# Kernel tuning notes

Measured on AMD Instinct MI355X. Metric: run time of the kernel, lower is better.

Reference implementation:

```python
import jax, jax.numpy as jnp
import numpy as np

B, C, F = 8, 2048, 128


def setup_inputs() -> dict:
    key = jax.random.key(0)
    ks = jax.random.split(key, 13)
    features = jax.random.normal(ks[0], (B, C, F), dtype=jnp.float32)
    # sparse-ish boolean adjacency masks over operations
    pred_mask = jax.random.uniform(ks[1], (B, C, C)) < 0.05
    succ_mask = jax.random.uniform(ks[2], (B, C, C)) < 0.05
    same_type_mask = jax.random.uniform(ks[3], (B, C, C)) < 0.10

    def linear(k, fan_in, fan_out):
        kw, kb = jax.random.split(k)
        bound = 1.0 / np.sqrt(fan_in)
        W = jax.random.uniform(kw, (fan_in, fan_out), minval=-bound, maxval=bound, dtype=jnp.float32)
        b = jax.random.uniform(kb, (fan_out,), minval=-bound, maxval=bound, dtype=jnp.float32)
        return W, b

    W_enc, b_enc = linear(ks[4], F, 4 * F)
    W_space, b_space = linear(ks[5], 3 * F, F)
    W_same, b_same = linear(ks[6], 2 * F, F)
    W_mix, b_mix = linear(ks[7], 2 * F, F)
    return {
        "features": features,
        "pred_mask": pred_mask,
        "succ_mask": succ_mask,
        "same_type_mask": same_type_mask,
        "W_enc": W_enc, "b_enc": b_enc,
        "W_space": W_space, "b_space": b_space,
        "W_same": W_same, "b_same": b_same,
        "W_mix": W_mix, "b_mix": b_mix,
    }


def reference(features, pred_mask, succ_mask, same_type_mask,
              W_enc, b_enc, W_space, b_space, W_same, b_same, W_mix, b_mix):
    # encoder: [B,C,F] -> [B,C,4F], split into origin + 3 message features
    enc = features @ W_enc + b_enc
    origin, e_pred, e_succ, e_same = jnp.split(enc, 4, axis=-1)

    def masked_mean(mask, e):
        # original builds (B,C,C,F) broadcast product then sums over 'other';
        # mathematically this is mask @ e with a clamped-degree divisor.
        m = mask.astype(e.dtype)                         # [B,C,C]
        deg = jnp.maximum(m.sum(-1, keepdims=True), 1.0)  # [B,C,1]
        return jnp.einsum('bij,bjf->bif', m, e) / deg

    pred_f = masked_mean(pred_mask, e_pred)
    succ_f = masked_mean(succ_mask, e_succ)
    same_f = masked_mean(same_type_mask, e_same)

    space_mixed = jnp.concatenate([pred_f, origin, succ_f], axis=-1) @ W_space + b_space
    same_mixed = jnp.concatenate([origin, same_f], axis=-1) @ W_same + b_same
    return jnp.concatenate([space_mixed, same_mixed], axis=-1) @ W_mix + b_mix
```

## Files before the change

### kernel.cpp

```cpp
#include <hip/hip_runtime.h>
#include <stdint.h>

typedef unsigned int uint;
typedef unsigned short ushort;
typedef unsigned char uchar;
typedef __attribute__((ext_vector_type(8))) short bf16x8;
typedef __attribute__((ext_vector_type(4))) float f32x4;

__device__ __forceinline__ ushort f2bf(float f) {
  uint u = __builtin_bit_cast(uint, f);
  return (ushort)((u + 0x7FFFu + ((u >> 16) & 1u)) >> 16);
}

__device__ __forceinline__ bf16x8 cvt8(uint lo, uint hi, uint& cacc) {
  uint x0 = __builtin_amdgcn_perm(0u, lo, 0x04010400u);
  uint x1 = __builtin_amdgcn_perm(0u, lo, 0x04030402u);
  uint x2 = __builtin_amdgcn_perm(0u, hi, 0x04010400u);
  uint x3 = __builtin_amdgcn_perm(0u, hi, 0x04030402u);
  uint n0 = ((x0 + 0x00FF00FFu) >> 8) & 0x00010001u;
  uint n1 = ((x1 + 0x00FF00FFu) >> 8) & 0x00010001u;
  uint n2 = ((x2 + 0x00FF00FFu) >> 8) & 0x00010001u;
  uint n3 = ((x3 + 0x00FF00FFu) >> 8) & 0x00010001u;
  cacc += n0 + n1 + n2 + n3;
  uint4 o;
  o.x = n0 * 0x3F80u; o.y = n1 * 0x3F80u;
  o.z = n2 * 0x3F80u; o.w = n3 * 0x3F80u;
  return __builtin_bit_cast(bf16x8, o);
}

__device__ __forceinline__ bf16x8 cvt8w(uint4 a, uint4 b, uint& cnt) {
  bf16x8 r;
  r[0] = a.x ? (short)0x3F80 : (short)0; cnt += (a.x != 0u);
  r[1] = a.y ? (short)0x3F80 : (short)0; cnt += (a.y != 0u);
  r[2] = a.z ? (short)0x3F80 : (short)0; cnt += (a.z != 0u);
  r[3] = a.w ? (short)0x3F80 : (short)0; cnt += (a.w != 0u);
  r[4] = b.x ? (short)0x3F80 : (short)0; cnt += (b.x != 0u);
  r[5] = b.y ? (short)0x3F80 : (short)0; cnt += (b.y != 0u);
  r[6] = b.z ? (short)0x3F80 : (short)0; cnt += (b.z != 0u);
  r[7] = b.w ? (short)0x3F80 : (short)0; cnt += (b.w != 0u);
  return r;
}

__global__ __launch_bounds__(256) void k_detect(
    const uint4* __restrict__ m, int* __restrict__ esz_out) {
  __shared__ int s_ok;
  if (threadIdx.x == 0) s_ok = 1;
  __syncthreads();
  int ok = 1;
#pragma unroll
  for (int i = 0; i < 16; ++i) {
    uint4 v = m[i * 256 + threadIdx.x];
    if (!(v.x <= 1u || v.x == 0x3F800000u)) ok = 0;
    if (!(v.y <= 1u || v.y == 0x3F800000u)) ok = 0;
    if (!(v.z <= 1u || v.z == 0x3F800000u)) ok = 0;
    if (!(v.w <= 1u || v.w == 0x3F800000u)) ok = 0;
  }
  if (!ok) atomicAnd(&s_ok, 0);
  __syncthreads();
  if (threadIdx.x == 0) *esz_out = s_ok ? 4 : 1;
}

__global__ __launch_bounds__(256) void k_prep(
    const float4* __restrict__ fin, ushort* __restrict__ fout,
    const float* __restrict__ We, const float* __restrict__ Ws,
    const float* __restrict__ Wm, const float* __restrict__ Wx,
    ushort* __restrict__ Te, ushort* __restrict__ Ts,
    ushort* __restrict__ Tm, ushort* __restrict__ Tx) {
  const int tid = blockIdx.x * 256 + threadIdx.x;
  for (int i = tid; i < 524288; i += 180224) {
    float4 v = fin[i];
    ushort4 o;
    o.x = f2bf(v.x); o.y = f2bf(v.y); o.z = f2bf(v.z); o.w = f2bf(v.w);
    *(ushort4*)&fout[(size_t)i * 4] = o;
  }
  int i = tid;
  if (i < 65536) { int n = i >> 7, k = i & 127; Te[i] = f2bf(We[k * 512 + n]); return; }
  i -= 65536;
  if (i < 49152) { int n = i / 384, k = i - n * 384; Ts[i] = f2bf(Ws[k * 128 + n]); return; }
  i -= 49152;
  if (i < 32768) { int n = i >> 8, k = i & 255; Tm[i] = f2bf(Wm[k * 128 + n]); return; }
  i -= 32768;
  if (i < 32768) { int n = i >> 8, k = i & 255; Tx[i] = f2bf(Wx[k * 128 + n]); return; }
}

__global__ __launch_bounds__(256) void k_enc(
    const ushort* __restrict__ featbf, const ushort* __restrict__ WTe,
    const float* __restrict__ bias, ushort* __restrict__ origin,
    ushort* __restrict__ eT0, ushort* __restrict__ eT1, ushort* __restrict__ eT2) {
  const int t = threadIdx.x;
  const int gm0 = blockIdx.x * 64;
  const int y = blockIdx.y;
  const int lane = t & 63, wave = t >> 6;
  const int m0w = (wave >> 1) * 32, n0w = (wave & 1) * 64;
  const int quad = lane >> 4, lr = lane & 15;
  const ushort* a0p = featbf + (size_t)(gm0 + m0w + lr) * 128 + quad * 8;
  const ushort* a1p = a0p + 16 * 128;
  bf16x8 af0[4], af1[4];
#pragma unroll
  for (int kc = 0; kc < 4; ++kc) {
    af0[kc] = *(const bf16x8*)(a0p + kc * 32);
    af1[kc] = *(const bf16x8*)(a1p + kc * 32);
  }
  f32x4 acc[2][4] = {};
#pragma unroll
  for (int j = 0; j < 4; ++j) {
    const ushort* bp = WTe + (size_t)(y * 128 + n0w + j * 16 + lr) * 128 + quad * 8;
#pragma unroll
    for (int kc = 0; kc < 4; ++kc) {
      bf16x8 bv = *(const bf16x8*)(bp + kc * 32);
      acc[0][j] = __builtin_amdgcn_mfma_f32_16x16x32_bf16(af0[kc], bv, acc[0][j], 0, 0, 0);
      acc[1][j] = __builtin_amdgcn_mfma_f32_16x16x32_bf16(af1[kc], bv, acc[1][j], 0, 0, 0);
    }
  }
  if (y == 0) {
#pragma unroll
    for (int i = 0; i < 2; ++i)
#pragma unroll
      for (int j = 0; j < 4; ++j) {
        int n = n0w + j * 16 + lr;
        float bb = bias[n];
        int mb = gm0 + m0w + i * 16 + quad * 4;
#pragma unroll
        for (int r = 0; r < 4; ++r)
          origin[(size_t)(mb + r) * 128 + n] = f2bf(acc[i][j][r] + bb);
      }
  } else {
    ushort* eT = (y == 1) ? eT0 : (y == 2) ? eT1 : eT2;
#pragma unroll
    for (int i = 0; i < 2; ++i)
#pragma unroll
      for (int j = 0; j < 4; ++j) {
        int n = n0w + j * 16 + lr;
        float bb = bias[y * 128 + n];
        int mb = gm0 + m0w + i * 16 + quad * 4;
        ushort4 o;
        o.x = f2bf(acc[i][j][0] + bb);
        o.y = f2bf(acc[i][j][1] + bb);
        o.z = f2bf(acc[i][j][2] + bb);
        o.w = f2bf(acc[i][j][3] + bb);
        *(ushort4*)&eT[(size_t)n * 16384 + mb] = o;
      }
  }
}

__global__ __launch_bounds__(256, 3) void k_mm(
    const void* __restrict__ mp, const void* __restrict__ ms,
    const void* __restrict__ mt,
    const ushort* __restrict__ eT0, const ushort* __restrict__ eT1,
    const ushort* __restrict__ eT2,
    ushort* __restrict__ P, ushort* __restrict__ S, ushort* __restrict__ T,
    const int* __restrict__ esz_p) {
  __shared__ uint degs[64];
  const int t = threadIdx.x;
  const int mtile = blockIdx.x, b = blockIdx.y, mid = blockIdx.z;
  const void* mask = (mid == 0) ? mp : (mid == 1) ? ms : mt;
  const ushort* eT = (mid == 0) ? eT0 : (mid == 1) ? eT1 : eT2;
  ushort* outp = (mid == 0) ? P : (mid == 1) ? S : T;
  const int esz = *esz_p;
  const size_t rowbase = (size_t)b * 2048 + mtile * 64;
  const int lane = t & 63, wave = t >> 6;
  const int m0w = (wave >> 1) * 32, n0w = (wave & 1) * 64;
  const int quad = lane >> 4, lr = lane & 15;
  const int r0 = m0w + lr, r1 = m0w + 16 + lr;
  const ushort* bp0 = eT + (size_t)(n0w + lr) * 16384 + (size_t)b * 2048 + quad * 8;
  const ushort* bp1 = bp0 + 16 * 16384;
  const ushort* bp2 = bp0 + 32 * 16384;
  const ushort* bp3 = bp0 + 48 * 16384;
  f32x4 acc[2][4] = {};
  uint cacc0 = 0, cacc1 = 0;

  if (esz == 1) {
    const uchar* ma = (const uchar*)mask + (rowbase + r0) * 2048 + quad * 8;
    const uchar* mb = (const uchar*)mask + (rowbase + r1) * 2048 + quad * 8;
    uint2 ra0 = *(const uint2*)(ma);
    uint2 ra1 = *(const uint2*)(ma + 32);
    uint2 rb0 = *(const uint2*)(mb);
    uint2 rb1 = *(const uint2*)(mb + 32);
#pragma unroll 2
    for (int k0 = 0; k0 < 2048; k0 += 64) {
      uint2 na0 = {}, na1 = {}, nb0 = {}, nb1 = {};
      if (k0 + 64 < 2048) {
        na0 = *(const uint2*)(ma + k0 + 64);
        na1 = *(const uint2*)(ma + k0 + 96);
        nb0 = *(const uint2*)(mb + k0 + 64);
        nb1 = *(const uint2*)(mb + k0 + 96);
      }
#pragma unroll
      for (int kc = 0; kc < 2; ++kc) {
        bf16x8 bv0 = *(const bf16x8*)(bp0 + k0 + kc * 32);
        bf16x8 bv1 = *(const bf16x8*)(bp1 + k0 + kc * 32);
        bf16x8 bv2 = *(const bf16x8*)(bp2 + k0 + kc * 32);
        bf16x8 bv3 = *(const bf16x8*)(bp3 + k0 + kc * 32);
        uint2 wa = kc ? ra1 : ra0;
        uint2 wb = kc ? rb1 : rb0;
        bf16x8 a0 = cvt8(wa.x, wa.y, cacc0);
        bf16x8 a1 = cvt8(wb.x, wb.y, cacc1);
        acc[0][0] = __builtin_amdgcn_mfma_f32_16x16x32_bf16(a0, bv0, acc[0][0], 0, 0, 0);
        acc[1][0] = __builtin_amdgcn_mfma_f32_16x16x32_bf16(a1, bv0, acc[1][0], 0, 0, 0);
        acc[0][1] = __builtin_amdgcn_mfma_f32_16x16x32_bf16(a0, bv1, acc[0][1], 0, 0, 0);
        acc[1][1] = __builtin_amdgcn_mfma_f32_16x16x32_bf16(a1, bv1, acc[1][1], 0, 0, 0);
        acc[0][2] = __builtin_amdgcn_mfma_f32_16x16x32_bf16(a0, bv2, acc[0][2], 0, 0, 0);
        acc[1][2] = __builtin_amdgcn_mfma_f32_16x16x32_bf16(a1, bv2, acc[1][2], 0, 0, 0);
        acc[0][3] = __builtin_amdgcn_mfma_f32_16x16x32_bf16(a0, bv3, acc[0][3], 0, 0, 0);
        acc[1][3] = __builtin_amdgcn_mfma_f32_16x16x32_bf16(a1, bv3, acc[1][3], 0, 0, 0);
      }
      ra0 = na0; ra1 = na1; rb0 = nb0; rb1 = nb1;
    }
  } else {
    const uint* ma = (const uint*)mask + (rowbase + r0) * 2048 + quad * 8;
    const uint* mb = (const uint*)mask + (rowbase + r1) * 2048 + quad * 8;
    for (int k0 = 0; k0 < 2048; k0 += 64) {
#pragma unroll
      for (int kc = 0; kc < 2; ++kc) {
        uint4 wa0 = *(const uint4*)(ma + k0 + kc * 32);
        uint4 wa1 = *(const uint4*)(ma + k0 + kc * 32 + 4);
        uint4 wb0 = *(const uint4*)(mb + k0 + kc * 32);
        uint4 wb1 = *(const uint4*)(mb + k0 + kc * 32 + 4);
        bf16x8 bv0 = *(const bf16x8*)(bp0 + k0 + kc * 32);
        bf16x8 bv1 = *(const bf16x8*)(bp1 + k0 + kc * 32);
        bf16x8 bv2 = *(const bf16x8*)(bp2 + k0 + kc * 32);
        bf16x8 bv3 = *(const bf16x8*)(bp3 + k0 + kc * 32);
        bf16x8 a0 = cvt8w(wa0, wa1, cacc0);
        bf16x8 a1 = cvt8w(wb0, wb1, cacc1);
        acc[0][0] = __builtin_amdgcn_mfma_f32_16x16x32_bf16(a0, bv0, acc[0][0], 0, 0, 0);
        acc[1][0] = __builtin_amdgcn_mfma_f32_16x16x32_bf16(a1, bv0, acc[1][0], 0, 0, 0);
        acc[0][1] = __builtin_amdgcn_mfma_f32_16x16x32_bf16(a0, bv1, acc[0][1], 0, 0, 0);
        acc[1][1] = __builtin_amdgcn_mfma_f32_16x16x32_bf16(a1, bv1, acc[1][1], 0, 0, 0);
        acc[0][2] = __builtin_amdgcn_mfma_f32_16x16x32_bf16(a0, bv2, acc[0][2], 0, 0, 0);
        acc[1][2] = __builtin_amdgcn_mfma_f32_16x16x32_bf16(a1, bv2, acc[1][2], 0, 0, 0);
        acc[0][3] = __builtin_amdgcn_mfma_f32_16x16x32_bf16(a0, bv3, acc[0][3], 0, 0, 0);
        acc[1][3] = __builtin_amdgcn_mfma_f32_16x16x32_bf16(a1, bv3, acc[1][3], 0, 0, 0);
      }
    }
  }

  int c0, c1;
  if (esz == 1) {
    c0 = (int)((cacc0 & 0xFFFFu) + (cacc0 >> 16));
    c1 = (int)((cacc1 & 0xFFFFu) + (cacc1 >> 16));
  } else {
    c0 = (int)cacc0;
    c1 = (int)cacc1;
  }
  c0 += __shfl_xor(c0, 16); c0 += __shfl_xor(c0, 32);
  c1 += __shfl_xor(c1, 16); c1 += __shfl_xor(c1, 32);
  if ((wave & 1) == 0 && quad == 0) { degs[r0] = (uint)c0; degs[r1] = (uint)c1; }
  __syncthreads();

#pragma unroll
  for (int i = 0; i < 2; ++i)
#pragma unroll
    for (int r = 0; r < 4; ++r) {
      int ml = m0w + i * 16 + quad * 4 + r;
      uint d = degs[ml];
      float inv = 1.0f / (float)(d > 0u ? d : 1u);
#pragma unroll
      for (int j = 0; j < 4; ++j) {
        int n = n0w + j * 16 + lr;
        outp[(rowbase + ml) * 128 + n] = f2bf(acc[i][j][r] * inv);
      }
    }
}

__device__ __forceinline__ void gemm_body(
    const ushort* __restrict__ A0, const ushort* __restrict__ A1,
    const ushort* __restrict__ A2, const ushort* __restrict__ Bsrc,
    int bstride, int K, const float* __restrict__ bias,
    void* __restrict__ out, int out_f32, int gm0, int t) {
  const int lane = t & 63, wave = t >> 6;
  const int m0w = (wave >> 1) * 32, n0w = (wave & 1) * 64;
  const int quad = lane >> 4, lr = lane & 15;
  const ushort* bbase = Bsrc + (size_t)(n0w + lr) * bstride + quad * 8;
  f32x4 acc[2][4] = {};
  for (int k0 = 0; k0 < K; k0 += 64) {
    const int seg = k0 >> 7;
    const ushort* Ap = (seg == 0) ? A0 : (seg == 1) ? A1 : A2;
    const int ko = k0 & 127;
    const ushort* a0p = Ap + (size_t)(gm0 + m0w + lr) * 128 + ko + quad * 8;
    const ushort* a1p = a0p + 16 * 128;
#pragma unroll
    for (int kc = 0; kc < 2; ++kc) {
      bf16x8 av0 = *(const bf16x8*)(a0p + kc * 32);
      bf16x8 av1 = *(const bf16x8*)(a1p + kc * 32);
      bf16x8 b0 = *(const bf16x8*)(bbase + k0 + kc * 32);
      bf16x8 b1 = *(const bf16x8*)(bbase + (size_t)16 * bstride + k0 + kc * 32);
      bf16x8 b2 = *(const bf16x8*)(bbase + (size_t)32 * bstride + k0 + kc * 32);
      bf16x8 b3 = *(const bf16x8*)(bbase + (size_t)48 * bstride + k0 + kc * 32);
      acc[0][0] = __builtin_amdgcn_mfma_f32_16x16x32_bf16(av0, b0, acc[0][0], 0, 0, 0);
      acc[1][0] = __builtin_amdgcn_mfma_f32_16x16x32_bf16(av1, b0, acc[1][0], 0, 0, 0);
      acc[0][1] = __builtin_amdgcn_mfma_f32_16x16x32_bf16(av0, b1, acc[0][1], 0, 0, 0);
      acc[1][1] = __builtin_amdgcn_mfma_f32_16x16x32_bf16(av1, b1, acc[1][1], 0, 0, 0);
      acc[0][2] = __builtin_amdgcn_mfma_f32_16x16x32_bf16(av0, b2, acc[0][2], 0, 0, 0);
      acc[1][2] = __builtin_amdgcn_mfma_f32_16x16x32_bf16(av1, b2, acc[1][2], 0, 0, 0);
      acc[0][3] = __builtin_amdgcn_mfma_f32_16x16x32_bf16(av0, b3, acc[0][3], 0, 0, 0);
      acc[1][3] = __builtin_amdgcn_mfma_f32_16x16x32_bf16(av1, b3, acc[1][3], 0, 0, 0);
    }
  }
#pragma unroll
  for (int i = 0; i < 2; ++i)
#pragma unroll
    for (int j = 0; j < 4; ++j) {
      const int n = n0w + j * 16 + lr;
      const float bb = bias[n];
      const int mb = gm0 + m0w + i * 16 + quad * 4;
      if (out_f32) {
#pragma unroll
        for (int r = 0; r < 4; ++r)
          ((float*)out)[(size_t)(mb + r) * 128 + n] = acc[i][j][r] + bb;
      } else {
#pragma unroll
        for (int r = 0; r < 4; ++r)
          ((ushort*)out)[(size_t)(mb + r) * 128 + n] = f2bf(acc[i][j][r] + bb);
      }
    }
}

__global__ __launch_bounds__(256) void k_xy(
    const ushort* __restrict__ P, const ushort* __restrict__ origin,
    const ushort* __restrict__ S, const ushort* __restrict__ T,
    const ushort* __restrict__ WTs, const ushort* __restrict__ WTm,
    const float* __restrict__ bs, const float* __restrict__ bm,
    ushort* __restrict__ X, ushort* __restrict__ Y) {
  const int gm0 = blockIdx.x * 64;
  if (blockIdx.y == 0)
    gemm_body(P, origin, S, WTs, 384, 384, bs, X, 0, gm0, threadIdx.x);
  else
    gemm_body(origin, T, nullptr, WTm, 256, 256, bm, Y, 0, gm0, threadIdx.x);
}

__global__ __launch_bounds__(256) void k_mix(
    const ushort* __restrict__ X, const ushort* __restrict__ Y,
    const ushort* __restrict__ WTx, const float* __restrict__ bx,
    float* __restrict__ out) {
  gemm_body(X, Y, nullptr, WTx, 256, 256, bx, out, 1, blockIdx.x * 64, threadIdx.x);
}

extern "C" void kernel_launch(void* const* d_in, const int* in_sizes, int n_in,
                              void* d_out, int out_size, void* d_ws,
                              size_t ws_size, hipStream_t stream) {
  const float* features = (const float*)d_in[0];
  const void* pred = d_in[1];
  const void* succ = d_in[2];
  const void* same = d_in[3];
  const float* W_enc = (const float*)d_in[4];
  const float* b_enc = (const float*)d_in[5];
  const float* W_space = (const float*)d_in[6];
  const float* b_space = (const float*)d_in[7];
  const float* W_same = (const float*)d_in[8];
  const float* b_same = (const float*)d_in[9];
  const float* W_mix = (const float*)d_in[10];
  const float* b_mix = (const float*)d_in[11];

  const size_t M = 16384;
  ushort* w = (ushort*)d_ws;
  ushort* feat_bf = w;  w += M * 128;
  ushort* WT_enc = w;   w += 512 * 128;
  ushort* WT_space = w; w += 128 * 384;
  ushort* WT_same = w;  w += 128 * 256;
  ushort* WT_mix = w;   w += 128 * 256;
  ushort* origin = w;   w += M * 128;
  ushort* eT0 = w;      w += M * 128;
  ushort* eT1 = w;      w += M * 128;
  ushort* eT2 = w;      w += M * 128;
  ushort* P = w;        w += M * 128;
  ushort* S = w;        w += M * 128;
  ushort* T = w;        w += M * 128;
  ushort* X = w;        w += M * 128;
  ushort* Y = w;        w += M * 128;
  int* esz = (int*)w;

  k_detect<<<1, 256, 0, stream>>>((const uint4*)pred, esz);
  k_prep<<<704, 256, 0, stream>>>((const float4*)features, feat_bf,
                                  W_enc, W_space, W_same, W_mix,
                                  WT_enc, WT_space, WT_same, WT_mix);
  k_enc<<<dim3(256, 4), 256, 0, stream>>>(feat_bf, WT_enc, b_enc,
                                          origin, eT0, eT1, eT2);
  k_mm<<<dim3(32, 8, 3), 256, 0, stream>>>(pred, succ, same, eT0, eT1, eT2,
                                           P, S, T, esz);
  k_xy<<<dim3(256, 2), 256, 0, stream>>>(P, origin, S, T, WT_space, WT_same,
                                         b_space, b_same, X, Y);
  k_mix<<<256, 256, 0, stream>>>(X, Y, WT_mix, b_mix, (float*)d_out);
}
```

Baseline: 500.3 us.

## Bit-pack masks with precomputed degrees and stage tiled operands via LDS in masked matmul

A new kernel packs each boolean or float adjacency mask into a 1-bit-per-entry tiled layout and precomputes the inverse degrees. The encoder now writes the message features as pre-swizzled K-step tiles through shared memory. The masked matmul then streams the packed mask and feature tiles into LDS with asynchronous global-to-LDS loads and double buffering, and expands bits to bf16 in registers. This targets the repeated wide mask reads and uncoalesced feature reads inside the matmul. The cost is an extra pass over the masks and a more intricate barrier and waitcnt pipeline. The packed buffer reuses the X/Y workspace region.

```diff
diff --git a/kernel.cpp b/kernel.cpp
--- a/kernel.cpp
+++ b/kernel.cpp
@@ -12,32 +12,20 @@
   return (ushort)((u + 0x7FFFu + ((u >> 16) & 1u)) >> 16);
 }
 
-__device__ __forceinline__ bf16x8 cvt8(uint lo, uint hi, uint& cacc) {
-  uint x0 = __builtin_amdgcn_perm(0u, lo, 0x04010400u);
-  uint x1 = __builtin_amdgcn_perm(0u, lo, 0x04030402u);
-  uint x2 = __builtin_amdgcn_perm(0u, hi, 0x04010400u);
-  uint x3 = __builtin_amdgcn_perm(0u, hi, 0x04030402u);
-  uint n0 = ((x0 + 0x00FF00FFu) >> 8) & 0x00010001u;
-  uint n1 = ((x1 + 0x00FF00FFu) >> 8) & 0x00010001u;
-  uint n2 = ((x2 + 0x00FF00FFu) >> 8) & 0x00010001u;
-  uint n3 = ((x3 + 0x00FF00FFu) >> 8) & 0x00010001u;
-  cacc += n0 + n1 + n2 + n3;
-  uint4 o;
-  o.x = n0 * 0x3F80u; o.y = n1 * 0x3F80u;
-  o.z = n2 * 0x3F80u; o.w = n3 * 0x3F80u;
-  return __builtin_bit_cast(bf16x8, o);
-}
-
-__device__ __forceinline__ bf16x8 cvt8w(uint4 a, uint4 b, uint& cnt) {
+__device__ __forceinline__ uint nz4(uint x) {
+  uint y = (x & 0x7F7F7F7Fu) + 0x7F7F7F7Fu;
+  uint z = (y | x) & 0x80808080u;
+  return ((z >> 7) & 1u) | ((z >> 14) & 2u) | ((z >> 21) & 4u) | ((z >> 28) & 8u);
+}
+__device__ __forceinline__ uint nzd4(uint4 v) {
+  return (uint)(v.x != 0u) | ((uint)(v.y != 0u) << 1) |
+         ((uint)(v.z != 0u) << 2) | ((uint)(v.w != 0u) << 3);
+}
+__device__ __forceinline__ bf16x8 bits2bf(uint byte) {
   bf16x8 r;
-  r[0] = a.x ? (short)0x3F80 : (short)0; cnt += (a.x != 0u);
-  r[1] = a.y ? (short)0x3F80 : (short)0; cnt += (a.y != 0u);
-  r[2] = a.z ? (short)0x3F80 : (short)0; cnt += (a.z != 0u);
-  r[3] = a.w ? (short)0x3F80 : (short)0; cnt += (a.w != 0u);
-  r[4] = b.x ? (short)0x3F80 : (short)0; cnt += (b.x != 0u);
-  r[5] = b.y ? (short)0x3F80 : (short)0; cnt += (b.y != 0u);
-  r[6] = b.z ? (short)0x3F80 : (short)0; cnt += (b.z != 0u);
-  r[7] = b.w ? (short)0x3F80 : (short)0; cnt += (b.w != 0u);
+#pragma unroll
+  for (int e = 0; e < 8; ++e)
+    r[e] = (short)(ushort)(((byte >> e) & 1u) ? 0x3F80u : 0u);
   return r;
 }
 
@@ -83,10 +71,58 @@
   if (i < 32768) { int n = i >> 8, k = i & 255; Tx[i] = f2bf(Wx[k * 128 + n]); return; }
 }
 
+__global__ __launch_bounds__(256) void k_maskpack(
+    const void* __restrict__ mp, const void* __restrict__ ms,
+    const void* __restrict__ mt, uchar* __restrict__ pk,
+    float* __restrict__ invdeg, const int* __restrict__ esz_p) {
+  const int t = threadIdx.x;
+  const int rg = blockIdx.x;
+  const int y = blockIdx.y;
+  const int mid = y >> 3, b = y & 7;
+  const void* mask = (mid == 0) ? mp : (mid == 1) ? ms : mt;
+  const int esz = *esz_p;
+  const int rl = t >> 5, seg = t & 31;
+  const int r = rg * 8 + rl;
+  uint lo, hi;
+  if (esz == 1) {
+    const uint4* p = (const uint4*)((const uchar*)mask +
+                                    ((size_t)b * 2048 + r) * 2048 + seg * 64);
+    uint4 v0 = p[0], v1 = p[1], v2 = p[2], v3 = p[3];
+    uint q0 = nz4(v0.x) | (nz4(v0.y) << 4) | (nz4(v0.z) << 8) | (nz4(v0.w) << 12);
+    uint q1 = nz4(v1.x) | (nz4(v1.y) << 4) | (nz4(v1.z) << 8) | (nz4(v1.w) << 12);
+    uint q2 = nz4(v2.x) | (nz4(v2.y) << 4) | (nz4(v2.z) << 8) | (nz4(v2.w) << 12);
+    uint q3 = nz4(v3.x) | (nz4(v3.y) << 4) | (nz4(v3.z) << 8) | (nz4(v3.w) << 12);
+    lo = q0 | (q1 << 16);
+    hi = q2 | (q3 << 16);
+  } else {
+    const uint4* p = (const uint4*)mask + ((size_t)b * 2048 + r) * 512 + seg * 16;
+    uint q[4];
+#pragma unroll
+    for (int g = 0; g < 4; ++g) {
+      uint4 w0 = p[g * 4 + 0], w1 = p[g * 4 + 1];
+      uint4 w2 = p[g * 4 + 2], w3 = p[g * 4 + 3];
+      q[g] = nzd4(w0) | (nzd4(w1) << 4) | (nzd4(w2) << 8) | (nzd4(w3) << 12);
+    }
+    lo = q[0] | (q[1] << 16);
+    hi = q[2] | (q[3] << 16);
+  }
+  int cnt = __popc(lo) + __popc(hi);
+#pragma unroll
+  for (int o = 1; o < 32; o <<= 1) cnt += __shfl_xor(cnt, o);
+  if (seg == 0)
+    invdeg[((size_t)mid * 8 + b) * 2048 + r] =
+        1.0f / (float)(cnt > 0 ? cnt : 1);
+  const int mtile = r >> 6, rowin = r & 63;
+  uint2 w2v; w2v.x = lo; w2v.y = hi;
+  *(uint2*)(pk + (((((size_t)(mid * 8 + b)) * 32 + mtile) * 32 + seg) * 64 +
+                  rowin) * 8) = w2v;
+}
+
 __global__ __launch_bounds__(256) void k_enc(
     const ushort* __restrict__ featbf, const ushort* __restrict__ WTe,
     const float* __restrict__ bias, ushort* __restrict__ origin,
-    ushort* __restrict__ eT0, ushort* __restrict__ eT1, ushort* __restrict__ eT2) {
+    ushort* __restrict__ eTt0, ushort* __restrict__ eTt1, ushort* __restrict__ eTt2) {
+  __shared__ ushort tr[128 * 64];
   const int t = threadIdx.x;
   const int gm0 = blockIdx.x * 64;
   const int y = blockIdx.y;
@@ -125,139 +161,132 @@
           origin[(size_t)(mb + r) * 128 + n] = f2bf(acc[i][j][r] + bb);
       }
   } else {
-    ushort* eT = (y == 1) ? eT0 : (y == 2) ? eT1 : eT2;
 #pragma unroll
     for (int i = 0; i < 2; ++i)
 #pragma unroll
       for (int j = 0; j < 4; ++j) {
         int n = n0w + j * 16 + lr;
         float bb = bias[y * 128 + n];
-        int mb = gm0 + m0w + i * 16 + quad * 4;
+        int m_lo = m0w + i * 16 + quad * 4;
+        int chunk = m_lo >> 3;
+        int byteo = n * 128 + ((chunk ^ (n & 7)) << 4) + (m_lo & 7) * 2;
         ushort4 o;
         o.x = f2bf(acc[i][j][0] + bb);
         o.y = f2bf(acc[i][j][1] + bb);
         o.z = f2bf(acc[i][j][2] + bb);
         o.w = f2bf(acc[i][j][3] + bb);
-        *(ushort4*)&eT[(size_t)n * 16384 + mb] = o;
+        *(ushort4*)((char*)tr + byteo) = o;
       }
+    __syncthreads();
+    ushort* eT = (y == 1) ? eTt0 : (y == 2) ? eTt1 : eTt2;
+    const int bb_ = blockIdx.x >> 5, kstep = blockIdx.x & 31;
+    uint4* dst = (uint4*)(eT + ((size_t)(bb_ * 32 + kstep)) * 8192);
+    const uint4* src = (const uint4*)tr;
+#pragma unroll
+    for (int ii = 0; ii < 4; ++ii) dst[ii * 256 + t] = src[ii * 256 + t];
   }
 }
 
 __global__ __launch_bounds__(256, 3) void k_mm(
-    const void* __restrict__ mp, const void* __restrict__ ms,
-    const void* __restrict__ mt,
-    const ushort* __restrict__ eT0, const ushort* __restrict__ eT1,
-    const ushort* __restrict__ eT2,
-    ushort* __restrict__ P, ushort* __restrict__ S, ushort* __restrict__ T,
-    const int* __restrict__ esz_p) {
-  __shared__ uint degs[64];
+    const uchar* __restrict__ pk, const float* __restrict__ invdeg,
+    const ushort* __restrict__ B0p, const ushort* __restrict__ B1p,
+    const ushort* __restrict__ B2p,
+    ushort* __restrict__ P, ushort* __restrict__ S, ushort* __restrict__ T) {
+  __shared__ __align__(16) char smem[49152];
   const int t = threadIdx.x;
-  const int mtile = blockIdx.x, b = blockIdx.y, mid = blockIdx.z;
-  const void* mask = (mid == 0) ? mp : (mid == 1) ? ms : mt;
-  const ushort* eT = (mid == 0) ? eT0 : (mid == 1) ? eT1 : eT2;
+  const int g = blockIdx.x;
+  const int X = g & 7, seq = g >> 3;
+  const int pl = seq >> 5, mtile = seq & 31;
+  const int panel = pl * 8 + X;
+  const int b = panel / 3, mid = panel - b * 3;
+  const ushort* Bt = (mid == 0) ? B0p : (mid == 1) ? B1p : B2p;
   ushort* outp = (mid == 0) ? P : (mid == 1) ? S : T;
-  const int esz = *esz_p;
-  const size_t rowbase = (size_t)b * 2048 + mtile * 64;
+  const uchar* pkT = pk + ((((size_t)(mid * 8 + b)) * 32 + mtile) * 32) * 512;
+  const uchar* BtT = (const uchar*)Bt + ((size_t)b * 32) * 16384;
   const int lane = t & 63, wave = t >> 6;
   const int m0w = (wave >> 1) * 32, n0w = (wave & 1) * 64;
   const int quad = lane >> 4, lr = lane & 15;
-  const int r0 = m0w + lr, r1 = m0w + 16 + lr;
-  const ushort* bp0 = eT + (size_t)(n0w + lr) * 16384 + (size_t)b * 2048 + quad * 8;
-  const ushort* bp1 = bp0 + 16 * 16384;
-  const ushort* bp2 = bp0 + 32 * 16384;
-  const ushort* bp3 = bp0 + 48 * 16384;
   f32x4 acc[2][4] = {};
-  uint cacc0 = 0, cacc1 = 0;
-
-  if (esz == 1) {
-    const uchar* ma = (const uchar*)mask + (rowbase + r0) * 2048 + quad * 8;
-    const uchar* mb = (const uchar*)mask + (rowbase + r1) * 2048 + quad * 8;
-    uint2 ra0 = *(const uint2*)(ma);
-    uint2 ra1 = *(const uint2*)(ma + 32);
-    uint2 rb0 = *(const uint2*)(mb);
-    uint2 rb1 = *(const uint2*)(mb + 32);
-#pragma unroll 2
-    for (int k0 = 0; k0 < 2048; k0 += 64) {
-      uint2 na0 = {}, na1 = {}, nb0 = {}, nb1 = {};
-      if (k0 + 64 < 2048) {
-        na0 = *(const uint2*)(ma + k0 + 64);
-        na1 = *(const uint2*)(ma + k0 + 96);
-        nb0 = *(const uint2*)(mb + k0 + 64);
-        nb1 = *(const uint2*)(mb + k0 + 96);
-      }
-#pragma unroll
-      for (int kc = 0; kc < 2; ++kc) {
-        bf16x8 bv0 = *(const bf16x8*)(bp0 + k0 + kc * 32);
-        bf16x8 bv1 = *(const bf16x8*)(bp1 + k0 + kc * 32);
-        bf16x8 bv2 = *(const bf16x8*)(bp2 + k0 + kc * 32);
-        bf16x8 bv3 = *(const bf16x8*)(bp3 + k0 + kc * 32);
-        uint2 wa = kc ? ra1 : ra0;
-        uint2 wb = kc ? rb1 : rb0;
-        bf16x8 a0 = cvt8(wa.x, wa.y, cacc0);
-        bf16x8 a1 = cvt8(wb.x, wb.y, cacc1);
-        acc[0][0] = __builtin_amdgcn_mfma_f32_16x16x32_bf16(a0, bv0, acc[0][0], 0, 0, 0);
-        acc[1][0] = __builtin_amdgcn_mfma_f32_16x16x32_bf16(a1, bv0, acc[1][0], 0, 0, 0);
-        acc[0][1] = __builtin_amdgcn_mfma_f32_16x16x32_bf16(a0, bv1, acc[0][1], 0, 0, 0);
-        acc[1][1] = __builtin_amdgcn_mfma_f32_16x16x32_bf16(a1, bv1, acc[1][1], 0, 0, 0);
-        acc[0][2] = __builtin_amdgcn_mfma_f32_16x16x32_bf16(a0, bv2, acc[0][2], 0, 0, 0);
-        acc[1][2] = __builtin_amdgcn_mfma_f32_16x16x32_bf16(a1, bv2, acc[1][2], 0, 0, 0);
-        acc[0][3] = __builtin_amdgcn_mfma_f32_16x16x32_bf16(a0, bv3, acc[0][3], 0, 0, 0);
-        acc[1][3] = __builtin_amdgcn_mfma_f32_16x16x32_bf16(a1, bv3, acc[1][3], 0, 0, 0);
-      }
-      ra0 = na0; ra1 = na1; rb0 = nb0; rb1 = nb1;
-    }
-  } else {
-    const uint* ma = (const uint*)mask + (rowbase + r0) * 2048 + quad * 8;
-    const uint* mb = (const uint*)mask + (rowbase + r1) * 2048 + quad * 8;
-    for (int k0 = 0; k0 < 2048; k0 += 64) {
-#pragma unroll
-      for (int kc = 0; kc < 2; ++kc) {
-        uint4 wa0 = *(const uint4*)(ma + k0 + kc * 32);
-        uint4 wa1 = *(const uint4*)(ma + k0 + kc * 32 + 4);
-        uint4 wb0 = *(const uint4*)(mb + k0 + kc * 32);
-        uint4 wb1 = *(const uint4*)(mb + k0 + kc * 32 + 4);
-        bf16x8 bv0 = *(const bf16x8*)(bp0 + k0 + kc * 32);
-        bf16x8 bv1 = *(const bf16x8*)(bp1 + k0 + kc * 32);
-        bf16x8 bv2 = *(const bf16x8*)(bp2 + k0 + kc * 32);
-        bf16x8 bv3 = *(const bf16x8*)(bp3 + k0 + kc * 32);
-        bf16x8 a0 = cvt8w(wa0, wa1, cacc0);
-        bf16x8 a1 = cvt8w(wb0, wb1, cacc1);
-        acc[0][0] = __builtin_amdgcn_mfma_f32_16x16x32_bf16(a0, bv0, acc[0][0], 0, 0, 0);
-        acc[1][0] = __builtin_amdgcn_mfma_f32_16x16x32_bf16(a1, bv0, acc[1][0], 0, 0, 0);
-        acc[0][1] = __builtin_amdgcn_mfma_f32_16x16x32_bf16(a0, bv1, acc[0][1], 0, 0, 0);
-        acc[1][1] = __builtin_amdgcn_mfma_f32_16x16x32_bf16(a1, bv1, acc[1][1], 0, 0, 0);
-        acc[0][2] = __builtin_amdgcn_mfma_f32_16x16x32_bf16(a0, bv2, acc[0][2], 0, 0, 0);
-        acc[1][2] = __builtin_amdgcn_mfma_f32_16x16x32_bf16(a1, bv2, acc[1][2], 0, 0, 0);
-        acc[0][3] = __builtin_amdgcn_mfma_f32_16x16x32_bf16(a0, bv3, acc[0][3], 0, 0, 0);
-        acc[1][3] = __builtin_amdgcn_mfma_f32_16x16x32_bf16(a1, bv3, acc[1][3], 0, 0, 0);
-      }
-    }
-  }
-
-  int c0, c1;
-  if (esz == 1) {
-    c0 = (int)((cacc0 & 0xFFFFu) + (cacc0 >> 16));
-    c1 = (int)((cacc1 & 0xFFFFu) + (cacc1 >> 16));
-  } else {
-    c0 = (int)cacc0;
-    c1 = (int)cacc1;
-  }
-  c0 += __shfl_xor(c0, 16); c0 += __shfl_xor(c0, 32);
-  c1 += __shfl_xor(c1, 16); c1 += __shfl_xor(c1, 32);
-  if ((wave & 1) == 0 && quad == 0) { degs[r0] = (uint)c0; degs[r1] = (uint)c1; }
-  __syncthreads();
-
+
+#define STG_A()                                                               \
+  {                                                                           \
+    _Pragma("unroll") for (int ii = 0; ii < 4; ++ii)                          \
+        __builtin_amdgcn_global_load_lds(                                     \
+            (const __attribute__((address_space(1))) uint*)(pkT +             \
+                wave * 4096 + ii * 1024 + lane * 16),                         \
+            (__attribute__((address_space(3))) uint*)(smem + wave * 4096 +    \
+                ii * 1024 + lane * 16),                                       \
+            16, 0, 0);                                                        \
+  }
+#define STG_B(BUF, STEP)                                                      \
+  {                                                                           \
+    _Pragma("unroll") for (int ii = 0; ii < 4; ++ii)                          \
+        __builtin_amdgcn_global_load_lds(                                     \
+            (const __attribute__((address_space(1))) uint*)(BtT +             \
+                (size_t)(STEP) * 16384 + wave * 4096 + ii * 1024 + lane * 16),\
+            (__attribute__((address_space(3))) uint*)(smem + 16384 +          \
+                (BUF) * 16384 + wave * 4096 + ii * 1024 + lane * 16),         \
+            16, 0, 0);                                                        \
+  }
+#define CPT(SS, BUF)                                                          \
+  {                                                                           \
+    const char* Ab = smem;                                                    \
+    const char* Bb = smem + 16384 + (BUF) * 16384;                            \
+    uint2 wa = *(const uint2*)(Ab + (SS) * 512 + (m0w + lr) * 8);             \
+    uint2 wb = *(const uint2*)(Ab + (SS) * 512 + (m0w + 16 + lr) * 8);        \
+    _Pragma("unroll") for (int kc = 0; kc < 2; ++kc) {                        \
+      uint wax = kc ? wa.y : wa.x;                                            \
+      uint wbx = kc ? wb.y : wb.x;                                            \
+      bf16x8 a0 = bits2bf((wax >> (quad * 8)) & 0xFFu);                       \
+      bf16x8 a1 = bits2bf((wbx >> (quad * 8)) & 0xFFu);                       \
+      const int sl = (((kc * 4 + quad) ^ (lr & 7)) << 4);                     \
+      bf16x8 b0 = *(const bf16x8*)(Bb + (n0w + lr) * 128 + sl);               \
+      bf16x8 b1 = *(const bf16x8*)(Bb + (n0w + 16 + lr) * 128 + sl);          \
+      bf16x8 b2 = *(const bf16x8*)(Bb + (n0w + 32 + lr) * 128 + sl);          \
+      bf16x8 b3 = *(const bf16x8*)(Bb + (n0w + 48 + lr) * 128 + sl);          \
+      __builtin_amdgcn_s_setprio(1);                                          \
+      acc[0][0] = __builtin_amdgcn_mfma_f32_16x16x32_bf16(a0, b0, acc[0][0], 0, 0, 0); \
+      acc[1][0] = __builtin_amdgcn_mfma_f32_16x16x32_bf16(a1, b0, acc[1][0], 0, 0, 0); \
+      acc[0][1] = __builtin_amdgcn_mfma_f32_16x16x32_bf16(a0, b1, acc[0][1], 0, 0, 0); \
+      acc[1][1] = __builtin_amdgcn_mfma_f32_16x16x32_bf16(a1, b1, acc[1][1], 0, 0, 0); \
+      acc[0][2] = __builtin_amdgcn_mfma_f32_16x16x32_bf16(a0, b2, acc[0][2], 0, 0, 0); \
+      acc[1][2] = __builtin_amdgcn_mfma_f32_16x16x32_bf16(a1, b2, acc[1][2], 0, 0, 0); \
+      acc[0][3] = __builtin_amdgcn_mfma_f32_16x16x32_bf16(a0, b3, acc[0][3], 0, 0, 0); \
+      acc[1][3] = __builtin_amdgcn_mfma_f32_16x16x32_bf16(a1, b3, acc[1][3], 0, 0, 0); \
+      __builtin_amdgcn_s_setprio(0);                                          \
+    }                                                                         \
+  }
+
+  STG_A()
+  STG_B(0, 0)
+  STG_B(1, 1)
+  for (int s = 0; s < 32; ++s) {
+    if (s < 31) asm volatile("s_waitcnt vmcnt(4)" ::: "memory");
+    else        asm volatile("s_waitcnt vmcnt(0)" ::: "memory");
+    __builtin_amdgcn_s_barrier();
+    __builtin_amdgcn_sched_barrier(0);
+    CPT(s, s & 1)
+    asm volatile("" ::: "memory");
+    __builtin_amdgcn_s_barrier();
+    if (s < 30) STG_B(s & 1, s + 2)
+  }
+  __builtin_amdgcn_sched_barrier(0);
+#undef CPT
+#undef STG_B
+#undef STG_A
+
+  const size_t rowbase = (size_t)b * 2048 + mtile * 64;
+  const float* inv = invdeg + ((size_t)(mid * 8 + b)) * 2048 + mtile * 64;
 #pragma unroll
   for (int i = 0; i < 2; ++i)
 #pragma unroll
     for (int r = 0; r < 4; ++r) {
       int ml = m0w + i * 16 + quad * 4 + r;
-      uint d = degs[ml];
-      float inv = 1.0f / (float)(d > 0u ? d : 1u);
+      float iv = inv[ml];
 #pragma unroll
       for (int j = 0; j < 4; ++j) {
         int n = n0w + j * 16 + lr;
-        outp[(rowbase + ml) * 128 + n] = f2bf(acc[i][j][r] * inv);
+        outp[(rowbase + ml) * 128 + n] = f2bf(acc[i][j][r] * iv);
       }
     }
 }
@@ -359,24 +388,27 @@
   ushort* WT_same = w;  w += 128 * 256;
   ushort* WT_mix = w;   w += 128 * 256;
   ushort* origin = w;   w += M * 128;
-  ushort* eT0 = w;      w += M * 128;
-  ushort* eT1 = w;      w += M * 128;
-  ushort* eT2 = w;      w += M * 128;
+  ushort* eTt0 = w;     w += M * 128;
+  ushort* eTt1 = w;     w += M * 128;
+  ushort* eTt2 = w;     w += M * 128;
   ushort* P = w;        w += M * 128;
   ushort* S = w;        w += M * 128;
   ushort* T = w;        w += M * 128;
-  ushort* X = w;        w += M * 128;
-  ushort* Y = w;        w += M * 128;
+  uchar* pk = (uchar*)w;
+  ushort* X = w;
+  ushort* Y = w + M * 128;
+  w += 6291456;
+  float* invdeg = (float*)w;  w += 98304;
   int* esz = (int*)w;
 
   k_detect<<<1, 256, 0, stream>>>((const uint4*)pred, esz);
   k_prep<<<704, 256, 0, stream>>>((const float4*)features, feat_bf,
                                   W_enc, W_space, W_same, W_mix,
                                   WT_enc, WT_space, WT_same, WT_mix);
+  k_maskpack<<<dim3(256, 24), 256, 0, stream>>>(pred, succ, same, pk, invdeg, esz);
   k_enc<<<dim3(256, 4), 256, 0, stream>>>(feat_bf, WT_enc, b_enc,
-                                          origin, eT0, eT1, eT2);
-  k_mm<<<dim3(32, 8, 3), 256, 0, stream>>>(pred, succ, same, eT0, eT1, eT2,
-                                           P, S, T, esz);
+                                          origin, eTt0, eTt1, eTt2);
+  k_mm<<<768, 256, 0, stream>>>(pk, invdeg, eTt0, eTt1, eTt2, P, S, T);
   k_xy<<<dim3(256, 2), 256, 0, stream>>>(P, origin, S, T, WT_space, WT_same,
                                          b_space, b_same, X, Y);
   k_mix<<<256, 256, 0, stream>>>(X, Y, WT_mix, b_mix, (float*)d_out);
```

Result: faster. 490.4 us (-2.0%).
